# Optimization experiments

Hardware: AMD Instinct MI355X
Metric: run time of the kernel (lower is better)

## Reference

```python
import jax, jax.numpy as jnp
import numpy as np

EMBED_DIM = 1024
NUM_HEADS = 8
HEAD_DIM = EMBED_DIM // NUM_HEADS


def setup_inputs() -> dict:
    key = jax.random.key(0)
    k1, k2, k3, k4, k5 = jax.random.split(key, 5)
    B, N, D = 4, 2048, EMBED_DIM
    scale = 1.0 / np.sqrt(D)
    return {
        "representation": jax.random.normal(k1, (B, N, D), dtype=jnp.float32),
        "W_qkv": jax.random.normal(k2, (D, 3 * D), dtype=jnp.float32) * scale,
        "b_qkv": jnp.zeros((3 * D,), dtype=jnp.float32),
        "W_proj": jax.random.normal(k3, (D, D), dtype=jnp.float32) * scale,
        "b_proj": jnp.zeros((D,), dtype=jnp.float32),
    }


def reference(representation, W_qkv, b_qkv, W_proj, b_proj):
    B, N, D = representation.shape
    H, Hd = NUM_HEADS, HEAD_DIM
    qkv = jnp.einsum("bnd,de->bne", representation, W_qkv) + b_qkv  # [B,N,3D]
    q, k, v = jnp.split(qkv, 3, axis=-1)
    # [B,N,D] -> [B,H,N,Hd]
    split_heads = lambda x: x.reshape(B, N, H, Hd).transpose(0, 2, 1, 3)
    q, k, v = split_heads(q), split_heads(k), split_heads(v)
    dots = jnp.einsum("bhqd,bhkd->bhqk", q, k) * (Hd ** -0.5)  # [B,H,N,N]
    attn = jax.nn.softmax(dots, axis=-1)
    out = jnp.einsum("bhqk,bhkd->bhqd", attn, v)
    out = out.transpose(0, 2, 1, 3).reshape(B, N, D)  # merge heads
    return jnp.einsum("bnd,de->bne", out, W_proj) + b_proj
```

## Files before the change

kernel.cpp:

```cpp
#include <hip/hip_runtime.h>
#include <hip/hip_bf16.h>
#include <cstdint>

typedef unsigned short u16;
typedef __attribute__((ext_vector_type(8))) short short8;
typedef __attribute__((ext_vector_type(4))) float f32x4;
typedef __attribute__((ext_vector_type(4))) unsigned short u16x4;
typedef __attribute__((ext_vector_type(4))) unsigned int u32x4;

#define NSEQ 2048
#define DMODEL 1024
#define NH 8
#define HD 128
#define KDIM 1024
#define QSCALE (0.08838834764831845f * 1.4426950408889634f)

__device__ __forceinline__ u16 f2b(float f) {
  __hip_bfloat16 h = __float2bfloat16(f);
  union { __hip_bfloat16 h; u16 u; } cv; cv.h = h; return cv.u;
}
__device__ __forceinline__ f32x4 zero4() { f32x4 z = {0.f, 0.f, 0.f, 0.f}; return z; }

__device__ __forceinline__ void gload_lds16(const u16* g, u16* l) {
  __builtin_amdgcn_global_load_lds(
      (__attribute__((address_space(1))) void*)g,
      (__attribute__((address_space(3))) void*)l, 16, 0, 0);
}

__device__ __forceinline__ int LK(int r) {
  return (r & 0x23) | ((r & 0x0C) << 1) | ((r & 0x10) >> 2);
}

__global__ void cvt_f32_bf16(const float* __restrict__ in, u16* __restrict__ out) {
  const size_t i = ((size_t)blockIdx.x * 256 + threadIdx.x) * 8;
  f32x4 a = *(const f32x4*)&in[i];
  f32x4 b = *(const f32x4*)&in[i + 4];
  short8 o;
#pragma unroll
  for (int j = 0; j < 4; ++j) { o[j] = (short)f2b(a[j]); o[4 + j] = (short)f2b(b[j]); }
  *(short8*)&out[i] = o;
}

__global__ void transpose_k(const float* __restrict__ in, u16* __restrict__ out,
                            int R, int C) {
  __shared__ u16 tile[32][33];
  const int tx = threadIdx.x, ty = threadIdx.y;
  const int c = blockIdx.x * 32 + tx;
  const int r0 = blockIdx.y * 32;
  for (int i = ty; i < 32; i += 8) tile[i][tx] = f2b(in[(size_t)(r0 + i) * C + c]);
  __syncthreads();
  const int oc = r0 + tx;
  const int c0 = blockIdx.x * 32;
  for (int i = ty; i < 32; i += 8) out[(size_t)(c0 + i) * R + oc] = tile[tx][i];
}

template <int MODE>
__global__ __launch_bounds__(256, 3) void gemm128(
    const u16* __restrict__ A, const u16* __restrict__ Bt,
    const float* __restrict__ bias, u16* __restrict__ o0,
    u16* __restrict__ o1, u16* __restrict__ o2, float* __restrict__ of) {
  __shared__ __align__(16) u16 sA[128 * 64];
  __shared__ __align__(16) u16 sB[128 * 64];

  const int tid = threadIdx.x;
  const int lane = tid & 63;
  const int w = tid >> 6;
  const int quad = lane >> 4, ln = lane & 15;
  const int m0 = blockIdx.y * 128, n0 = blockIdx.x * 128;
  const int wm = (w >> 1) * 64, wn = (w & 1) * 64;

  f32x4 acc[4][4];
#pragma unroll
  for (int i = 0; i < 4; ++i)
#pragma unroll
    for (int j = 0; j < 4; ++j) acc[i][j] = zero4();

  const int cbase = w * 4;
  for (int kb = 0; kb < KDIM / 64; ++kb) {
    __syncthreads();
    const int k0 = kb * 64;
#pragma unroll
    for (int i = 0; i < 4; ++i) {
      int c = (cbase + i) * 64 + lane;
      int r = c >> 3, s = c & 7;
      gload_lds16(A + (size_t)(m0 + r) * KDIM + k0 + s * 8, &sA[(cbase + i) * 512]);
      gload_lds16(Bt + (size_t)(n0 + r) * KDIM + k0 + s * 8, &sB[(cbase + i) * 512]);
    }
    __syncthreads();
#pragma unroll
    for (int ks = 0; ks < 2; ++ks) {
      short8 af[4], bf[4];
      const int kc = ks * 4 + quad;
#pragma unroll
      for (int t = 0; t < 4; ++t) {
        af[t] = *(const short8*)&sA[(wm + t * 16 + ln) * 64 + kc * 8];
        bf[t] = *(const short8*)&sB[(wn + t * 16 + ln) * 64 + kc * 8];
      }
#pragma unroll
      for (int mt = 0; mt < 4; ++mt)
#pragma unroll
        for (int nt = 0; nt < 4; ++nt)
          acc[mt][nt] = __builtin_amdgcn_mfma_f32_16x16x32_bf16(
              af[mt], bf[nt], acc[mt][nt], 0, 0, 0);
    }
  }

  if (MODE == 0) {
    const int which = n0 >> 10;
    const int h = (n0 & 1023) >> 7;
#pragma unroll
    for (int mt = 0; mt < 4; ++mt) {
      const int rbase = m0 + wm + mt * 16 + quad * 4;
      const int b = rbase >> 11;
      const int n = rbase & 2047;
#pragma unroll
      for (int nt = 0; nt < 4; ++nt) {
        const int dcol = wn + nt * 16 + ln;
        const float bv = bias[n0 + dcol];
        if (which == 0) {
          u16* p = o0 + ((size_t)(b * NH + h) * NSEQ + n) * HD + dcol;
#pragma unroll
          for (int rr = 0; rr < 4; ++rr)
            p[(size_t)rr * HD] = f2b((acc[mt][nt][rr] + bv) * QSCALE);
        } else if (which == 1) {
          u16* p = o1 + ((size_t)(b * NH + h) * NSEQ + n) * HD + dcol;
#pragma unroll
          for (int rr = 0; rr < 4; ++rr)
            p[(size_t)rr * HD] = f2b(acc[mt][nt][rr] + bv);
        } else {
          u16x4 pk;
#pragma unroll
          for (int rr = 0; rr < 4; ++rr) pk[rr] = f2b(acc[mt][nt][rr] + bv);
          *(u16x4*)&o2[((size_t)(b * NH + h) * HD + dcol) * NSEQ + n] = pk;
        }
      }
    }
  } else {
#pragma unroll
    for (int mt = 0; mt < 4; ++mt) {
      const int rbase = m0 + wm + mt * 16 + quad * 4;
#pragma unroll
      for (int nt = 0; nt < 4; ++nt) {
        const int col = n0 + wn + nt * 16 + ln;
        const float bv = bias[col];
#pragma unroll
        for (int rr = 0; rr < 4; ++rr)
          of[(size_t)(rbase + rr) * DMODEL + col] = acc[mt][nt][rr] + bv;
      }
    }
  }
}

__global__ __launch_bounds__(256, 2) void attn_fused(
    const u16* __restrict__ Q, const u16* __restrict__ K,
    const u16* __restrict__ Vt, u16* __restrict__ AO) {
  __shared__ __align__(16) u16 sK[2][64 * 128];

  const int tid = threadIdx.x;
  const int w = tid >> 6, lane = tid & 63;
  const int quad = lane >> 4, ln = lane & 15;
  const int bh = blockIdx.y;
  const int q0 = blockIdx.x * 128;

  const u16* Qb = Q + ((size_t)bh * NSEQ + q0) * HD;
  const u16* Kb = K + (size_t)bh * NSEQ * HD;
  const u16* Vb = Vt + (size_t)bh * HD * NSEQ;

  int gk_off[4];
#pragma unroll
  for (int j = 0; j < 4; ++j) {
    const int c = (w * 4 + j) * 64 + lane;
    const int rk = c >> 4, sk_ = c & 15;
    gk_off[j] = LK(rk) * HD + (sk_ ^ (rk & 7)) * 8;
  }

  int kbase[4], kslot[4];
#pragma unroll
  for (int n = 0; n < 4; ++n) kbase[n] = (n * 16 + ln) * 128;
#pragma unroll
  for (int ks = 0; ks < 4; ++ks)
    kslot[ks] = (((ks << 2) | quad) ^ (ln & 7)) * 8;

  const u16* vbase = Vb + (size_t)ln * NSEQ + quad * 8;

  short8 qf[2][4];
#pragma unroll
  for (int mt = 0; mt < 2; ++mt)
#pragma unroll
    for (int ks = 0; ks < 4; ++ks)
      qf[mt][ks] = *(const short8*)&Qb[(size_t)(w * 32 + mt * 16 + ln) * HD +
                                       ks * 32 + quad * 8];

  f32x4 o[2][8];
#pragma unroll
  for (int mt = 0; mt < 2; ++mt)
#pragma unroll
    for (int dt = 0; dt < 8; ++dt) o[mt][dt] = zero4();
  float l_part[2] = {0.f, 0.f};

#pragma unroll
  for (int j = 0; j < 4; ++j)
    gload_lds16(Kb + gk_off[j], &sK[0][(w * 4 + j) * 512]);

  union PU { u32x4 u; short8 s; };

#pragma unroll 1
  for (int it = 0; it < NSEQ / 128; ++it) {
#pragma unroll
    for (int c2 = 0; c2 < 2; ++c2) {
      const int kv = it * 128 + c2 * 64;
      __syncthreads();

      short8 vf[2][8];
#pragma unroll
      for (int dt = 0; dt < 8; ++dt)
        vf[0][dt] = *(const short8*)&vbase[(size_t)dt * 16 * NSEQ + kv];
#pragma unroll
      for (int dt = 0; dt < 8; ++dt)
        vf[1][dt] = *(const short8*)&vbase[(size_t)dt * 16 * NSEQ + kv + 32];

      const int kvn = kv + 64;
      if (kvn < NSEQ) {
#pragma unroll
        for (int j = 0; j < 4; ++j)
          gload_lds16(Kb + (size_t)kvn * HD + gk_off[j],
                      &sK[c2 ^ 1][(w * 4 + j) * 512]);
      }
      const u16* skr = &sK[c2][0];

      __builtin_amdgcn_s_setprio(1);

      f32x4 sacc[4][2];
      PU ph[2][2];

      auto SM = [&](int m) {
#pragma unroll
        for (int mt = 0; mt < 2; ++mt) {
          float e0 = exp2f(sacc[m][mt][0]);
          float e1 = exp2f(sacc[m][mt][1]);
          float e2 = exp2f(sacc[m][mt][2]);
          float e3 = exp2f(sacc[m][mt][3]);
          l_part[mt] += (e0 + e1) + (e2 + e3);
          unsigned a0 = __float_as_uint(e0) + 0x8000u;
          unsigned a1 = __float_as_uint(e1) + 0x8000u;
          unsigned a2 = __float_as_uint(e2) + 0x8000u;
          unsigned a3 = __float_as_uint(e3) + 0x8000u;
          ph[mt][m >> 1].u[(m & 1) * 2 + 0] = __builtin_amdgcn_perm(a1, a0, 0x07060302);
          ph[mt][m >> 1].u[(m & 1) * 2 + 1] = __builtin_amdgcn_perm(a3, a2, 0x07060302);
        }
      };

#pragma unroll
      for (int n = 0; n < 4; ++n) {
#pragma unroll
        for (int mt = 0; mt < 2; ++mt) sacc[n][mt] = zero4();
#pragma unroll
        for (int ks = 0; ks < 4; ++ks) {
          short8 kf = *(const short8*)&skr[kbase[n] + kslot[ks]];
          sacc[n][0] = __builtin_amdgcn_mfma_f32_16x16x32_bf16(
              kf, qf[0][ks], sacc[n][0], 0, 0, 0);
          sacc[n][1] = __builtin_amdgcn_mfma_f32_16x16x32_bf16(
              kf, qf[1][ks], sacc[n][1], 0, 0, 0);
        }
        if (n) SM(n - 1);
      }

      {
        short8 pf0 = ph[0][0].s, pf1 = ph[1][0].s;
#pragma unroll
        for (int dt = 0; dt < 8; ++dt) {
          o[0][dt] = __builtin_amdgcn_mfma_f32_16x16x32_bf16(
              pf0, vf[0][dt], o[0][dt], 0, 0, 0);
          o[1][dt] = __builtin_amdgcn_mfma_f32_16x16x32_bf16(
              pf1, vf[0][dt], o[1][dt], 0, 0, 0);
        }
      }
      SM(3);
      {
        short8 pf0 = ph[0][1].s, pf1 = ph[1][1].s;
#pragma unroll
        for (int dt = 0; dt < 8; ++dt) {
          o[0][dt] = __builtin_amdgcn_mfma_f32_16x16x32_bf16(
              pf0, vf[1][dt], o[0][dt], 0, 0, 0);
          o[1][dt] = __builtin_amdgcn_mfma_f32_16x16x32_bf16(
              pf1, vf[1][dt], o[1][dt], 0, 0, 0);
        }
      }
      __builtin_amdgcn_s_setprio(0);
    }
  }

  const int b = bh >> 3, h = bh & 7;
#pragma unroll
  for (int mt = 0; mt < 2; ++mt) {
    float v = l_part[mt];
    v += __shfl_xor(v, 16, 64);
    v += __shfl_xor(v, 32, 64);
    float inv[4];
#pragma unroll
    for (int rr = 0; rr < 4; ++rr)
      inv[rr] = 1.0f / __shfl(v, quad * 4 + rr, 64);
    const int rbase = q0 + w * 32 + mt * 16 + quad * 4;
#pragma unroll
    for (int dt = 0; dt < 8; ++dt) {
      const int d = dt * 16 + ln;
#pragma unroll
      for (int rr = 0; rr < 4; ++rr)
        AO[((size_t)b * NSEQ + rbase + rr) * DMODEL + h * HD + d] =
            f2b(o[mt][dt][rr] * inv[rr]);
    }
  }
}

extern "C" void kernel_launch(void* const* d_in, const int* in_sizes, int n_in,
                              void* d_out, int out_size, void* d_ws, size_t ws_size,
                              hipStream_t stream) {
  const float* X = (const float*)d_in[0];
  const float* Wqkv = (const float*)d_in[1];
  const float* bqkv = (const float*)d_in[2];
  const float* Wproj = (const float*)d_in[3];
  const float* bproj = (const float*)d_in[4];
  float* out = (float*)d_out;

  const size_t NEED_BYTES =
      2ull * (8388608  + 3072 * 1024 + 1024 * 1024 + 3 * 8388608 + 8388608);
  if (ws_size < NEED_BYTES) return;

  u16* ws = (u16*)d_ws;
  u16* Xb = ws;
  u16* WqkvT = Xb + 8388608;
  u16* WprojT = WqkvT + 3072 * 1024;
  u16* Qb = WprojT + 1024 * 1024;
  u16* Kb = Qb + 8388608;
  u16* Vtb = Kb + 8388608;
  u16* AO = Vtb + 8388608;

  cvt_f32_bf16<<<8388608 / (256 * 8), 256, 0, stream>>>(X, Xb);
  transpose_k<<<dim3(3072 / 32, 1024 / 32), dim3(32, 8), 0, stream>>>(Wqkv, WqkvT, 1024, 3072);
  transpose_k<<<dim3(1024 / 32, 1024 / 32), dim3(32, 8), 0, stream>>>(Wproj, WprojT, 1024, 1024);
  gemm128<0><<<dim3(3072 / 128, 8192 / 128), 256, 0, stream>>>(
      Xb, WqkvT, bqkv, Qb, Kb, Vtb, nullptr);
  attn_fused<<<dim3(2048 / 128, 32), 256, 0, stream>>>(Qb, Kb, Vtb, AO);
  gemm128<1><<<dim3(1024 / 128, 8192 / 128), 256, 0, stream>>>(
      AO, WprojT, bproj, nullptr, nullptr, nullptr, out);
}
```

Measured before the change: 326.1 us.

## Split attention KV across two blocks, stage V in LDS, swizzle GEMM grid

Attention now splits the key/value sequence into two halves along a new grid z dimension, which doubles the number of workgroups. Each half writes unnormalized bf16 partial outputs and row sums, and a new combine kernel adds them and normalizes. V tiles are now loaded into LDS via async global-to-LDS copies with a 32-key tile, and occupancy is raised to 4 blocks per CU. The GEMMs use a 1D grid remapped so neighbouring block IDs share the same output column tile, aiming for better cache reuse. The cost is an extra kernel pass over the output, an extra bf16 rounding of the partials, and reuse of dead workspace buffers (Xb, WqkvT) for the partials. The split halves are summed without per-half max rescaling, which matches the existing softmax that also subtracts no row max.

```diff
diff --git a/kernel.cpp b/kernel.cpp
--- a/kernel.cpp
+++ b/kernel.cpp
@@ -18,6 +18,9 @@
 __device__ __forceinline__ u16 f2b(float f) {
   __hip_bfloat16 h = __float2bfloat16(f);
   union { __hip_bfloat16 h; u16 u; } cv; cv.h = h; return cv.u;
+}
+__device__ __forceinline__ float b2f(u16 u) {
+  union { float f; unsigned v; } c; c.v = ((unsigned)u) << 16; return c.f;
 }
 __device__ __forceinline__ f32x4 zero4() { f32x4 z = {0.f, 0.f, 0.f, 0.f}; return z; }
 
@@ -66,7 +69,13 @@
   const int lane = tid & 63;
   const int w = tid >> 6;
   const int quad = lane >> 4, ln = lane & 15;
-  const int m0 = blockIdx.y * 128, n0 = blockIdx.x * 128;
+
+  const int NT = (MODE == 0) ? 24 : 8;
+  const int nwg = gridDim.x, cpx = nwg >> 3;
+  const int id = blockIdx.x;
+  const int swz = (id & 7) * cpx + (id >> 3);
+  const int m0 = (swz / NT) * 128, n0 = (swz % NT) * 128;
+
   const int wm = (w >> 1) * 64, wn = (w & 1) * 64;
 
   f32x4 acc[4][4];
@@ -151,37 +160,45 @@
   }
 }
 
-__global__ __launch_bounds__(256, 2) void attn_fused(
+__global__ __launch_bounds__(256, 4) void attn_fused(
     const u16* __restrict__ Q, const u16* __restrict__ K,
-    const u16* __restrict__ Vt, u16* __restrict__ AO) {
-  __shared__ __align__(16) u16 sK[2][64 * 128];
+    const u16* __restrict__ Vt, u16* __restrict__ OP0,
+    u16* __restrict__ OP1, float* __restrict__ Lp) {
+  __shared__ __align__(16) u16 sK[2][32 * 128];
+  __shared__ __align__(16) u16 sV[2][128 * 32];
 
   const int tid = threadIdx.x;
   const int w = tid >> 6, lane = tid & 63;
   const int quad = lane >> 4, ln = lane & 15;
   const int bh = blockIdx.y;
   const int q0 = blockIdx.x * 128;
+  const int s = blockIdx.z;
+  const int kv0 = s * (NSEQ / 2);
+  const int kvend = kv0 + NSEQ / 2;
 
   const u16* Qb = Q + ((size_t)bh * NSEQ + q0) * HD;
   const u16* Kb = K + (size_t)bh * NSEQ * HD;
   const u16* Vb = Vt + (size_t)bh * HD * NSEQ;
 
-  int gk_off[4];
-#pragma unroll
-  for (int j = 0; j < 4; ++j) {
-    const int c = (w * 4 + j) * 64 + lane;
+  int gk_off[2], gv_off[2];
+#pragma unroll
+  for (int j = 0; j < 2; ++j) {
+    const int c = j * 256 + w * 64 + lane;
     const int rk = c >> 4, sk_ = c & 15;
     gk_off[j] = LK(rk) * HD + (sk_ ^ (rk & 7)) * 8;
-  }
-
-  int kbase[4], kslot[4];
-#pragma unroll
-  for (int n = 0; n < 4; ++n) kbase[n] = (n * 16 + ln) * 128;
+    const int rv = c >> 2, sv_ = c & 3;
+    gv_off[j] = rv * NSEQ + (sv_ ^ (rv & 3)) * 8;
+  }
+
+  int kbase[2], kslot[4], vfo[8];
+#pragma unroll
+  for (int n = 0; n < 2; ++n) kbase[n] = (n * 16 + ln) * 128;
 #pragma unroll
   for (int ks = 0; ks < 4; ++ks)
     kslot[ks] = (((ks << 2) | quad) ^ (ln & 7)) * 8;
-
-  const u16* vbase = Vb + (size_t)ln * NSEQ + quad * 8;
+#pragma unroll
+  for (int dt = 0; dt < 8; ++dt)
+    vfo[dt] = (dt * 16 + ln) * 32 + ((quad ^ (ln & 3)) * 8);
 
   short8 qf[2][4];
 #pragma unroll
@@ -199,39 +216,37 @@
   float l_part[2] = {0.f, 0.f};
 
 #pragma unroll
-  for (int j = 0; j < 4; ++j)
-    gload_lds16(Kb + gk_off[j], &sK[0][(w * 4 + j) * 512]);
+  for (int j = 0; j < 2; ++j) {
+    gload_lds16(Kb + (size_t)kv0 * HD + gk_off[j], &sK[0][(j * 256 + w * 64) * 8]);
+    gload_lds16(Vb + kv0 + gv_off[j], &sV[0][(j * 256 + w * 64) * 8]);
+  }
 
   union PU { u32x4 u; short8 s; };
 
 #pragma unroll 1
-  for (int it = 0; it < NSEQ / 128; ++it) {
+  for (int it = 0; it < (NSEQ / 2) / 64; ++it) {
 #pragma unroll
     for (int c2 = 0; c2 < 2; ++c2) {
-      const int kv = it * 128 + c2 * 64;
+      const int kv = kv0 + (it * 2 + c2) * 32;
       __syncthreads();
 
-      short8 vf[2][8];
-#pragma unroll
-      for (int dt = 0; dt < 8; ++dt)
-        vf[0][dt] = *(const short8*)&vbase[(size_t)dt * 16 * NSEQ + kv];
-#pragma unroll
-      for (int dt = 0; dt < 8; ++dt)
-        vf[1][dt] = *(const short8*)&vbase[(size_t)dt * 16 * NSEQ + kv + 32];
-
-      const int kvn = kv + 64;
-      if (kvn < NSEQ) {
-#pragma unroll
-        for (int j = 0; j < 4; ++j)
+      const int kvn = kv + 32;
+      if (kvn < kvend) {
+#pragma unroll
+        for (int j = 0; j < 2; ++j) {
           gload_lds16(Kb + (size_t)kvn * HD + gk_off[j],
-                      &sK[c2 ^ 1][(w * 4 + j) * 512]);
+                      &sK[c2 ^ 1][(j * 256 + w * 64) * 8]);
+          gload_lds16(Vb + kvn + gv_off[j], &sV[c2 ^ 1][(j * 256 + w * 64) * 8]);
+        }
       }
       const u16* skr = &sK[c2][0];
+      const u16* svr = &sV[c2][0];
 
       __builtin_amdgcn_s_setprio(1);
 
-      f32x4 sacc[4][2];
-      PU ph[2][2];
+      f32x4 sacc[2][2];
+      PU ph[2];
+      short8 vf[8];
 
       auto SM = [&](int m) {
 #pragma unroll
@@ -245,71 +260,88 @@
           unsigned a1 = __float_as_uint(e1) + 0x8000u;
           unsigned a2 = __float_as_uint(e2) + 0x8000u;
           unsigned a3 = __float_as_uint(e3) + 0x8000u;
-          ph[mt][m >> 1].u[(m & 1) * 2 + 0] = __builtin_amdgcn_perm(a1, a0, 0x07060302);
-          ph[mt][m >> 1].u[(m & 1) * 2 + 1] = __builtin_amdgcn_perm(a3, a2, 0x07060302);
+          ph[mt].u[m * 2 + 0] = __builtin_amdgcn_perm(a1, a0, 0x07060302);
+          ph[mt].u[m * 2 + 1] = __builtin_amdgcn_perm(a3, a2, 0x07060302);
         }
       };
 
 #pragma unroll
-      for (int n = 0; n < 4; ++n) {
-#pragma unroll
-        for (int mt = 0; mt < 2; ++mt) sacc[n][mt] = zero4();
-#pragma unroll
-        for (int ks = 0; ks < 4; ++ks) {
-          short8 kf = *(const short8*)&skr[kbase[n] + kslot[ks]];
-          sacc[n][0] = __builtin_amdgcn_mfma_f32_16x16x32_bf16(
-              kf, qf[0][ks], sacc[n][0], 0, 0, 0);
-          sacc[n][1] = __builtin_amdgcn_mfma_f32_16x16x32_bf16(
-              kf, qf[1][ks], sacc[n][1], 0, 0, 0);
-        }
-        if (n) SM(n - 1);
-      }
-
-      {
-        short8 pf0 = ph[0][0].s, pf1 = ph[1][0].s;
-#pragma unroll
-        for (int dt = 0; dt < 8; ++dt) {
-          o[0][dt] = __builtin_amdgcn_mfma_f32_16x16x32_bf16(
-              pf0, vf[0][dt], o[0][dt], 0, 0, 0);
-          o[1][dt] = __builtin_amdgcn_mfma_f32_16x16x32_bf16(
-              pf1, vf[0][dt], o[1][dt], 0, 0, 0);
-        }
-      }
-      SM(3);
-      {
-        short8 pf0 = ph[0][1].s, pf1 = ph[1][1].s;
-#pragma unroll
-        for (int dt = 0; dt < 8; ++dt) {
-          o[0][dt] = __builtin_amdgcn_mfma_f32_16x16x32_bf16(
-              pf0, vf[1][dt], o[0][dt], 0, 0, 0);
-          o[1][dt] = __builtin_amdgcn_mfma_f32_16x16x32_bf16(
-              pf1, vf[1][dt], o[1][dt], 0, 0, 0);
-        }
+      for (int mt = 0; mt < 2; ++mt) sacc[0][mt] = zero4();
+#pragma unroll
+      for (int ks = 0; ks < 4; ++ks) {
+        short8 kf = *(const short8*)&skr[kbase[0] + kslot[ks]];
+        sacc[0][0] = __builtin_amdgcn_mfma_f32_16x16x32_bf16(
+            kf, qf[0][ks], sacc[0][0], 0, 0, 0);
+        sacc[0][1] = __builtin_amdgcn_mfma_f32_16x16x32_bf16(
+            kf, qf[1][ks], sacc[0][1], 0, 0, 0);
+      }
+#pragma unroll
+      for (int dt = 0; dt < 4; ++dt)
+        vf[dt] = *(const short8*)&svr[vfo[dt]];
+#pragma unroll
+      for (int mt = 0; mt < 2; ++mt) sacc[1][mt] = zero4();
+#pragma unroll
+      for (int ks = 0; ks < 4; ++ks) {
+        short8 kf = *(const short8*)&skr[kbase[1] + kslot[ks]];
+        sacc[1][0] = __builtin_amdgcn_mfma_f32_16x16x32_bf16(
+            kf, qf[0][ks], sacc[1][0], 0, 0, 0);
+        sacc[1][1] = __builtin_amdgcn_mfma_f32_16x16x32_bf16(
+            kf, qf[1][ks], sacc[1][1], 0, 0, 0);
+      }
+      SM(0);
+#pragma unroll
+      for (int dt = 4; dt < 8; ++dt)
+        vf[dt] = *(const short8*)&svr[vfo[dt]];
+      SM(1);
+
+#pragma unroll
+      for (int dt = 0; dt < 8; ++dt) {
+        o[0][dt] = __builtin_amdgcn_mfma_f32_16x16x32_bf16(
+            ph[0].s, vf[dt], o[0][dt], 0, 0, 0);
+        o[1][dt] = __builtin_amdgcn_mfma_f32_16x16x32_bf16(
+            ph[1].s, vf[dt], o[1][dt], 0, 0, 0);
       }
       __builtin_amdgcn_s_setprio(0);
     }
   }
 
+  u16* OP = (s == 0) ? OP0 : OP1;
   const int b = bh >> 3, h = bh & 7;
 #pragma unroll
   for (int mt = 0; mt < 2; ++mt) {
     float v = l_part[mt];
     v += __shfl_xor(v, 16, 64);
     v += __shfl_xor(v, 32, 64);
-    float inv[4];
-#pragma unroll
-    for (int rr = 0; rr < 4; ++rr)
-      inv[rr] = 1.0f / __shfl(v, quad * 4 + rr, 64);
+    if (quad == 0)
+      Lp[(size_t)s * 65536 + bh * NSEQ + q0 + w * 32 + mt * 16 + ln] = v;
     const int rbase = q0 + w * 32 + mt * 16 + quad * 4;
 #pragma unroll
     for (int dt = 0; dt < 8; ++dt) {
       const int d = dt * 16 + ln;
 #pragma unroll
       for (int rr = 0; rr < 4; ++rr)
-        AO[((size_t)b * NSEQ + rbase + rr) * DMODEL + h * HD + d] =
-            f2b(o[mt][dt][rr] * inv[rr]);
-    }
-  }
+        OP[((size_t)b * NSEQ + rbase + rr) * DMODEL + h * HD + d] =
+            f2b(o[mt][dt][rr]);
+    }
+  }
+}
+
+__global__ void combine_attn(const u16* __restrict__ P0, u16* AO,
+                             const float* __restrict__ Lp) {
+  const size_t i0 = ((size_t)blockIdx.x * 256 + threadIdx.x) * 8;
+  const int n = (int)((i0 >> 10) & 2047);
+  const int b = (int)(i0 >> 21);
+  const int h = (int)((i0 >> 7) & 7);
+  const int bh = b * NH + h;
+  const float l = Lp[bh * NSEQ + n] + Lp[65536 + bh * NSEQ + n];
+  const float inv = 1.0f / l;
+  short8 p0 = *(const short8*)&P0[i0];
+  short8 p1 = *(const short8*)&AO[i0];
+  short8 r;
+#pragma unroll
+  for (int j = 0; j < 8; ++j)
+    r[j] = (short)f2b((b2f((u16)p0[j]) + b2f((u16)p1[j])) * inv);
+  *(short8*)&AO[i0] = r;
 }
 
 extern "C" void kernel_launch(void* const* d_in, const int* in_sizes, int n_in,
@@ -338,9 +370,9 @@
   cvt_f32_bf16<<<8388608 / (256 * 8), 256, 0, stream>>>(X, Xb);
   transpose_k<<<dim3(3072 / 32, 1024 / 32), dim3(32, 8), 0, stream>>>(Wqkv, WqkvT, 1024, 3072);
   transpose_k<<<dim3(1024 / 32, 1024 / 32), dim3(32, 8), 0, stream>>>(Wproj, WprojT, 1024, 1024);
-  gemm128<0><<<dim3(3072 / 128, 8192 / 128), 256, 0, stream>>>(
-      Xb, WqkvT, bqkv, Qb, Kb, Vtb, nullptr);
-  attn_fused<<<dim3(2048 / 128, 32), 256, 0, stream>>>(Qb, Kb, Vtb, AO);
-  gemm128<1><<<dim3(1024 / 128, 8192 / 128), 256, 0, stream>>>(
-      AO, WprojT, bproj, nullptr, nullptr, nullptr, out);
-}
+  gemm128<0><<<1536, 256, 0, stream>>>(Xb, WqkvT, bqkv, Qb, Kb, Vtb, nullptr);
+  attn_fused<<<dim3(2048 / 128, 32, 2), 256, 0, stream>>>(
+      Qb, Kb, Vtb, Xb, AO, (float*)WqkvT);
+  combine_attn<<<8388608 / (256 * 8), 256, 0, stream>>>(Xb, AO, (const float*)WqkvT);
+  gemm128<1><<<512, 256, 0, stream>>>(AO, WprojT, bproj, nullptr, nullptr, nullptr, out);
+}
```

New measurement: 522.0 us. 60.1% more time.
